# Kernel optimization log

Measured on AMD Instinct MI355X. Metric: run time of the kernel, lower is better.

## Reference

```python
import jax, jax.numpy as jnp
import numpy as np

N_NODES = 150000
N_EDGES = 2400000
F_IN, HID, N_CLS = 22, 32, 6
BN_EPS = 1e-5


def setup_inputs() -> dict:
    key = jax.random.key(0)
    ks = jax.random.split(key, 10)
    x = jax.random.normal(ks[0], (N_NODES, F_IN), dtype=jnp.float32)
    edge_index = jax.random.randint(ks[1], (2, N_EDGES), 0, N_NODES, dtype=jnp.int64)
    # xavier-uniform style linear weights, zero biases (as in _init_weights)
    def xavier(k, fan_in, fan_out):
        lim = float(np.sqrt(6.0 / (fan_in + fan_out)))
        return jax.random.uniform(k, (fan_in, fan_out), jnp.float32, -lim, lim)
    return {
        "x": x,
        "edge_index": edge_index,
        "W_emb": xavier(ks[2], F_IN, HID),
        "b_emb": jnp.zeros((HID,), jnp.float32),
        "W_gcn": xavier(ks[3], HID, HID),
        "b_gcn": jnp.zeros((HID,), jnp.float32),
        "gamma": jnp.ones((HID,), jnp.float32),
        "beta": jnp.zeros((HID,), jnp.float32),
        "W_cls": xavier(ks[4], HID, N_CLS),
        "b_cls": jnp.zeros((N_CLS,), jnp.float32),
    }


def reference(x, edge_index, W_emb, b_emb, W_gcn, b_gcn, gamma, beta, W_cls, b_cls):
    N = x.shape[0]
    # embedding + relu
    h = jax.nn.relu(x @ W_emb + b_emb)                      # [N, HID]
    # GCNConv: linear transform first
    h = h @ W_gcn                                           # [N, HID]
    # add self-loops
    loops = jnp.arange(N, dtype=edge_index.dtype)
    src = jnp.concatenate([edge_index[0], loops])           # [E+N]
    dst = jnp.concatenate([edge_index[1], loops])
    # symmetric normalization deg^{-1/2} A_hat deg^{-1/2}
    deg = jax.ops.segment_sum(jnp.ones_like(dst, dtype=h.dtype), dst, num_segments=N)
    dis = jnp.where(deg > 0, jax.lax.rsqrt(jnp.where(deg > 0, deg, 1.0)), 0.0)
    norm = dis[src] * dis[dst]                              # [E+N]
    msg = h[src] * norm[:, None]                            # gather + scale
    agg = jax.ops.segment_sum(msg, dst, num_segments=N) + b_gcn
    # BatchNorm1d (training-mode batch statistics, biased variance)
    mean = jnp.mean(agg, axis=0)
    var = jnp.mean((agg - mean) ** 2, axis=0)
    hn = (agg - mean) * jax.lax.rsqrt(var + BN_EPS) * gamma + beta
    hn = jax.nn.relu(hn)
    # dropout is identity in eval; classifier
    return hn @ W_cls + b_cls
```

## Files before the change

kernel.cpp:

```cpp
#include <hip/hip_runtime.h>

#define N_NODES 150000
#define N_EDGES 2400000
#define F_IN    22
#define HID     32
#define N_CLS   6
#define BN_EPS  1e-5f

#define BSHIFT  8
#define BMASK   255
#define NB      ((N_NODES + BMASK) >> BSHIFT)
#define NBLK_BIN 256
#define CHUNK   ((N_EDGES + NBLK_BIN - 1) / NBLK_BIN)
#define CHUNK_H 8192
#define NBLK_H  ((N_EDGES + CHUNK_H - 1) / CHUNK_H)
#define EMB_NPB 64
#define NBLK_EMB ((N_NODES + EMB_NPB - 1) / EMB_NPB)
#define NREP    8

__device__ __forceinline__ unsigned bf16rne(float f) {
    unsigned u = __float_as_uint(f);
    return (u + 0x7FFFu + ((u >> 16) & 1u)) >> 16;
}
__device__ __forceinline__ float bflo(unsigned p) { return __uint_as_float(p << 16); }
__device__ __forceinline__ float bfhi(unsigned p) { return __uint_as_float(p & 0xFFFF0000u); }

__global__ void embed_hist_kernel(const float* __restrict__ x,
                                  const float* __restrict__ W_emb,
                                  const float* __restrict__ b_emb,
                                  const float* __restrict__ W_gcn,
                                  unsigned* __restrict__ hb,
                                  const int* __restrict__ dst,
                                  int* __restrict__ bcnt) {
    if (blockIdx.x < NBLK_EMB) {
        __shared__ float sWe[F_IN * HID];
        __shared__ float sbe[HID];
        __shared__ float sWg[HID * HID];
        __shared__ float sx[EMB_NPB * 23];
        __shared__ float sh1[EMB_NPB * 33];
        __shared__ unsigned sp[EMB_NPB * 17];
        for (int t = threadIdx.x; t < F_IN * HID; t += 256) sWe[t] = W_emb[t];
        if (threadIdx.x < HID) sbe[threadIdx.x] = b_emb[threadIdx.x];
        for (int t = threadIdx.x; t < HID * HID; t += 256) sWg[t] = W_gcn[t];

        int nbase = blockIdx.x * EMB_NPB;
        int nvalid = N_NODES - nbase; if (nvalid > EMB_NPB) nvalid = EMB_NPB;

        {
            const float* xg = x + (size_t)nbase * F_IN;
            int totalx = nvalid * F_IN;
            for (int L = threadIdx.x; L < totalx; L += 256)
                sx[(L / F_IN) * 23 + (L % F_IN)] = xg[L];
        }
        __syncthreads();

        int n = threadIdx.x >> 2;
        int q = threadIdx.x & 3;
        bool act = n < nvalid;

        if (act) {
#pragma unroll
            for (int j = 0; j < 8; ++j) {
                float acc = sbe[q * 8 + j];
#pragma unroll
                for (int f = 0; f < F_IN; ++f)
                    acc = fmaf(sx[n * 23 + f], sWe[f * HID + q * 8 + j], acc);
                sh1[n * 33 + q * 8 + j] = fmaxf(acc, 0.0f);
            }
        }
        __syncthreads();

        if (act) {
            float o[8];
#pragma unroll
            for (int j = 0; j < 8; ++j) o[j] = 0.0f;
#pragma unroll
            for (int f = 0; f < HID; ++f) {
                float hv = sh1[n * 33 + f];
#pragma unroll
                for (int j = 0; j < 8; ++j)
                    o[j] = fmaf(hv, sWg[f * HID + q * 8 + j], o[j]);
            }
#pragma unroll
            for (int jj = 0; jj < 4; ++jj)
                sp[n * 17 + q * 4 + jj] = bf16rne(o[2 * jj]) | (bf16rne(o[2 * jj + 1]) << 16);
        }
        __syncthreads();

        int total = nvalid * 16;
        size_t gbase = (size_t)nbase * 16;
        for (int L = threadIdx.x; L < total; L += 256)
            hb[gbase + L] = sp[(L >> 4) * 17 + (L & 15)];
    } else {
        __shared__ int hloc[NB];
        for (int t = threadIdx.x; t < NB; t += 256) hloc[t] = 0;
        __syncthreads();
        int base = (blockIdx.x - NBLK_EMB) * CHUNK_H;
        int end = base + CHUNK_H; if (end > N_EDGES) end = N_EDGES;
        for (int i = base + threadIdx.x; i < end; i += 256)
            atomicAdd(&hloc[dst[i] >> BSHIFT], 1);
        __syncthreads();
        for (int t = threadIdx.x; t < NB; t += 256)
            if (hloc[t]) atomicAdd(&bcnt[t], hloc[t]);
    }
}

__global__ void bucket_scan_kernel(const int* __restrict__ bcnt,
                                   int* __restrict__ boff,
                                   int* __restrict__ bcur,
                                   float* __restrict__ stats) {
    int t = threadIdx.x;
    if (t < 64 * NREP) stats[t] = 0.0f;
    __shared__ int s[1024];
    int v0 = (t < NB) ? bcnt[t] : 0;
    s[t] = v0;
    __syncthreads();
#pragma unroll
    for (int o = 1; o < 1024; o <<= 1) {
        int v = (t >= o) ? s[t - o] : 0;
        __syncthreads();
        s[t] += v;
        __syncthreads();
    }
    if (t < NB) {
        int e = s[t] - v0;
        boff[t] = e;
        bcur[t] = e;
    }
    if (t == NB - 1) boff[NB] = s[t];
}

__global__ void bin_edges_kernel(const int* __restrict__ src,
                                 const int* __restrict__ dst,
                                 int* __restrict__ bcur,
                                 unsigned int* __restrict__ binned) {
    __shared__ int hloc[NB];
    __shared__ int base[NB];
    __shared__ int lcur[NB];
    for (int t = threadIdx.x; t < NB; t += 512) hloc[t] = 0;
    __syncthreads();

    int cbase = blockIdx.x * CHUNK;
    int cend = cbase + CHUNK; if (cend > N_EDGES) cend = N_EDGES;
    for (int i = cbase + threadIdx.x; i < cend; i += 512)
        atomicAdd(&hloc[dst[i] >> BSHIFT], 1);
    __syncthreads();
    for (int t = threadIdx.x; t < NB; t += 512) {
        int c = hloc[t];
        base[t] = c ? atomicAdd(&bcur[t], c) : 0;
        lcur[t] = 0;
    }
    __syncthreads();
    for (int i = cbase + threadIdx.x; i < cend; i += 512) {
        int d = dst[i];
        int b = d >> BSHIFT;
        int r = atomicAdd(&lcur[b], 1);
        binned[base[b] + r] = ((unsigned)(d & BMASK) << 24) | (unsigned)src[i];
    }
}

__global__ void bucket_csr_kernel(const int* __restrict__ boff,
                                  const unsigned int* __restrict__ binned,
                                  int* __restrict__ sorted_src,
                                  int* __restrict__ off,
                                  float* __restrict__ dis) {
    __shared__ int s_cnt[256];
    __shared__ int s_scan[256];
    __shared__ int s_cur[256];
    int b = blockIdx.x;
    int t = threadIdx.x;
    int s0 = boff[b], s1 = boff[b + 1];
    int nbase = b << BSHIFT;
    int nnode = N_NODES - nbase; if (nnode > 256) nnode = 256;

    s_cnt[t] = 0;
    __syncthreads();
    for (int k = s0 + t; k < s1; k += 256)
        atomicAdd(&s_cnt[binned[k] >> 24], 1);
    __syncthreads();

    int v = s_cnt[t];
    s_scan[t] = v;
    __syncthreads();
#pragma unroll
    for (int o = 1; o < 256; o <<= 1) {
        int u = (t >= o) ? s_scan[t - o] : 0;
        __syncthreads();
        s_scan[t] += u;
        __syncthreads();
    }
    int excl = s_scan[t] - v;
    s_cur[t] = excl;
    if (t < nnode) {
        off[nbase + t] = s0 + excl;
        dis[nbase + t] = rsqrtf(1.0f + (float)v);
    }
    if (b == NB - 1 && t == 0) off[N_NODES] = N_EDGES;
    __syncthreads();

    for (int k = s0 + t; k < s1; k += 256) {
        unsigned p = binned[k];
        int n = (int)(p >> 24);
        int r = atomicAdd(&s_cur[n], 1);
        sorted_src[s0 + r] = (int)(p & 0xFFFFFFu);
    }
}

__global__ void aggregate_kernel(const int* __restrict__ off,
                                 const int* __restrict__ sorted_src,
                                 const unsigned* __restrict__ hb,
                                 const float* __restrict__ dis,
                                 float* __restrict__ agg,
                                 float* __restrict__ stats) {
    int t = blockIdx.x * blockDim.x + threadIdx.x;
    int node = t >> 3;
    int c = t & 7;
    bool active = node < N_NODES;

    float4 ps = {0.f, 0.f, 0.f, 0.f};
    float4 pq = {0.f, 0.f, 0.f, 0.f};

    if (active) {
        const uint2* hrow = reinterpret_cast<const uint2*>(hb);
        float dn = dis[node];
        uint2 hp = hrow[(size_t)node * 8 + c];
        float4 a0, a1, a2, a3;
        a0.x = bflo(hp.x) * dn; a0.y = bfhi(hp.x) * dn;
        a0.z = bflo(hp.y) * dn; a0.w = bfhi(hp.y) * dn;
        a1 = a2 = a3 = make_float4(0.f, 0.f, 0.f, 0.f);

        int b = off[node], e = off[node + 1];
        int k = b;
        for (; k + 8 <= e; k += 8) {
            int s0 = sorted_src[k],     s1 = sorted_src[k + 1];
            int s2 = sorted_src[k + 2], s3 = sorted_src[k + 3];
            int s4 = sorted_src[k + 4], s5 = sorted_src[k + 5];
            int s6 = sorted_src[k + 6], s7 = sorted_src[k + 7];
            float d0 = dis[s0], d1 = dis[s1], d2 = dis[s2], d3 = dis[s3];
            float d4 = dis[s4], d5 = dis[s5], d6 = dis[s6], d7 = dis[s7];
            uint2 v0 = hrow[(size_t)s0 * 8 + c];
            uint2 v1 = hrow[(size_t)s1 * 8 + c];
            uint2 v2 = hrow[(size_t)s2 * 8 + c];
            uint2 v3 = hrow[(size_t)s3 * 8 + c];
            uint2 v4 = hrow[(size_t)s4 * 8 + c];
            uint2 v5 = hrow[(size_t)s5 * 8 + c];
            uint2 v6 = hrow[(size_t)s6 * 8 + c];
            uint2 v7 = hrow[(size_t)s7 * 8 + c];
            a0.x = fmaf(bflo(v0.x), d0, a0.x); a0.y = fmaf(bfhi(v0.x), d0, a0.y);
            a0.z = fmaf(bflo(v0.y), d0, a0.z); a0.w = fmaf(bfhi(v0.y), d0, a0.w);
            a1.x = fmaf(bflo(v1.x), d1, a1.x); a1.y = fmaf(bfhi(v1.x), d1, a1.y);
            a1.z = fmaf(bflo(v1.y), d1, a1.z); a1.w = fmaf(bfhi(v1.y), d1, a1.w);
            a2.x = fmaf(bflo(v2.x), d2, a2.x); a2.y = fmaf(bfhi(v2.x), d2, a2.y);
            a2.z = fmaf(bflo(v2.y), d2, a2.z); a2.w = fmaf(bfhi(v2.y), d2, a2.w);
            a3.x = fmaf(bflo(v3.x), d3, a3.x); a3.y = fmaf(bfhi(v3.x), d3, a3.y);
            a3.z = fmaf(bflo(v3.y), d3, a3.z); a3.w = fmaf(bfhi(v3.y), d3, a3.w);
            a0.x = fmaf(bflo(v4.x), d4, a0.x); a0.y = fmaf(bfhi(v4.x), d4, a0.y);
            a0.z = fmaf(bflo(v4.y), d4, a0.z); a0.w = fmaf(bfhi(v4.y), d4, a0.w);
            a1.x = fmaf(bflo(v5.x), d5, a1.x); a1.y = fmaf(bfhi(v5.x), d5, a1.y);
            a1.z = fmaf(bflo(v5.y), d5, a1.z); a1.w = fmaf(bfhi(v5.y), d5, a1.w);
            a2.x = fmaf(bflo(v6.x), d6, a2.x); a2.y = fmaf(bfhi(v6.x), d6, a2.y);
            a2.z = fmaf(bflo(v6.y), d6, a2.z); a2.w = fmaf(bfhi(v6.y), d6, a2.w);
            a3.x = fmaf(bflo(v7.x), d7, a3.x); a3.y = fmaf(bfhi(v7.x), d7, a3.y);
            a3.z = fmaf(bflo(v7.y), d7, a3.z); a3.w = fmaf(bfhi(v7.y), d7, a3.w);
        }
        for (; k < e; ++k) {
            int s = sorted_src[k];
            float d = dis[s];
            uint2 v = hrow[(size_t)s * 8 + c];
            a0.x = fmaf(bflo(v.x), d, a0.x); a0.y = fmaf(bfhi(v.x), d, a0.y);
            a0.z = fmaf(bflo(v.y), d, a0.z); a0.w = fmaf(bfhi(v.y), d, a0.w);
        }
        float4 o;
        o.x = (a0.x + a1.x + a2.x + a3.x) * dn;
        o.y = (a0.y + a1.y + a2.y + a3.y) * dn;
        o.z = (a0.z + a1.z + a2.z + a3.z) * dn;
        o.w = (a0.w + a1.w + a2.w + a3.w) * dn;
        reinterpret_cast<float4*>(agg)[(size_t)node * 8 + c] = o;
        ps = o;
        pq.x = o.x * o.x; pq.y = o.y * o.y; pq.z = o.z * o.z; pq.w = o.w * o.w;
    }

    __shared__ float S[256 * 4];
    __shared__ float Q[256 * 4];
    S[threadIdx.x * 4 + 0] = ps.x; S[threadIdx.x * 4 + 1] = ps.y;
    S[threadIdx.x * 4 + 2] = ps.z; S[threadIdx.x * 4 + 3] = ps.w;
    Q[threadIdx.x * 4 + 0] = pq.x; Q[threadIdx.x * 4 + 1] = pq.y;
    Q[threadIdx.x * 4 + 2] = pq.z; Q[threadIdx.x * 4 + 3] = pq.w;
    __syncthreads();
    if (threadIdx.x < 32) {
        int cc = threadIdx.x >> 2, j = threadIdx.x & 3;
        float s = 0.0f, q = 0.0f;
#pragma unroll
        for (int w = 0; w < 32; ++w) {
            int tid = (w << 3) | cc;
            s += S[tid * 4 + j];
            q += Q[tid * 4 + j];
        }
        float* rep = stats + 64 * (blockIdx.x & (NREP - 1));
        atomicAdd(&rep[threadIdx.x], s);
        atomicAdd(&rep[32 + threadIdx.x], q);
    }
}

__global__ void cls_kernel(const float* __restrict__ agg,
                           const float* __restrict__ stats,
                           const float* __restrict__ gamma,
                           const float* __restrict__ beta,
                           const float* __restrict__ W_cls,
                           const float* __restrict__ b_cls,
                           float* __restrict__ out) {
    __shared__ float sA[HID];
    __shared__ float sB[HID];
    __shared__ float sW[HID * N_CLS];
    __shared__ float sb[N_CLS];
    if (threadIdx.x < HID) {
        float sum = 0.0f, sq = 0.0f;
#pragma unroll
        for (int r = 0; r < NREP; ++r) {
            sum += stats[r * 64 + threadIdx.x];
            sq  += stats[r * 64 + 32 + threadIdx.x];
        }
        const float invN = 1.0f / (float)N_NODES;
        float mean = sum * invN;
        float var = sq * invN - mean * mean;
        float inv = rsqrtf(var + BN_EPS);
        float A = gamma[threadIdx.x] * inv;
        sA[threadIdx.x] = A;
        sB[threadIdx.x] = beta[threadIdx.x] - mean * A;
    }
    for (int t = threadIdx.x; t < HID * N_CLS; t += blockDim.x) sW[t] = W_cls[t];
    if (threadIdx.x < N_CLS) sb[threadIdx.x] = b_cls[threadIdx.x];
    __syncthreads();

    int i = blockIdx.x * blockDim.x + threadIdx.x;
    if (i >= N_NODES) return;

    float acc[N_CLS];
#pragma unroll
    for (int c = 0; c < N_CLS; ++c) acc[c] = sb[c];
#pragma unroll
    for (int f = 0; f < HID; ++f) {
        float t = fmaxf(fmaf(agg[(size_t)i * HID + f], sA[f], sB[f]), 0.0f);
#pragma unroll
        for (int c = 0; c < N_CLS; ++c) acc[c] = fmaf(t, sW[f * N_CLS + c], acc[c]);
    }
#pragma unroll
    for (int c = 0; c < N_CLS; ++c) out[(size_t)i * N_CLS + c] = acc[c];
}

extern "C" void kernel_launch(void* const* d_in, const int* in_sizes, int n_in,
                              void* d_out, int out_size, void* d_ws, size_t ws_size,
                              hipStream_t stream) {
    const float* x     = (const float*)d_in[0];
    const int*   edge  = (const int*)d_in[1];
    const float* W_emb = (const float*)d_in[2];
    const float* b_emb = (const float*)d_in[3];
    const float* W_gcn = (const float*)d_in[4];
    const float* gamma = (const float*)d_in[6];
    const float* beta  = (const float*)d_in[7];
    const float* W_cls = (const float*)d_in[8];
    const float* b_cls = (const float*)d_in[9];
    float* out = (float*)d_out;

    unsigned*     hb         = (unsigned*)d_ws;
    float*        agg        = (float*)(hb + (size_t)N_NODES * HID / 2);
    float*        dis        = agg + (size_t)N_NODES * HID;
    int*          off        = (int*)(dis + N_NODES);
    int*          bcnt       = off + N_NODES + 1;
    int*          boff       = bcnt + NB;
    int*          bcur       = boff + NB + 1;
    unsigned int* binned     = (unsigned int*)(bcur + NB);
    int*          sorted_src = (int*)(binned + N_EDGES);
    float*        stats      = (float*)(sorted_src + N_EDGES);

    hipMemsetAsync(bcnt, 0, NB * sizeof(int), stream);

    const int* src = edge;
    const int* dst = edge + N_EDGES;

    embed_hist_kernel<<<NBLK_EMB + NBLK_H, 256, 0, stream>>>(x, W_emb, b_emb, W_gcn,
                                                             hb, dst, bcnt);
    bucket_scan_kernel<<<1, 1024, 0, stream>>>(bcnt, boff, bcur, stats);
    bin_edges_kernel<<<NBLK_BIN, 512, 0, stream>>>(src, dst, bcur, binned);
    bucket_csr_kernel<<<NB, 256, 0, stream>>>(boff, binned, sorted_src, off, dis);
    aggregate_kernel<<<(N_NODES * 8 + 255) / 256, 256, 0, stream>>>(off, sorted_src,
                                                                    hb, dis, agg, stats);
    cls_kernel<<<(N_NODES + 255) / 256, 256, 0, stream>>>(agg, stats, gamma, beta,
                                                          W_cls, b_cls, out);
}
```

Measured before the change: 154.0 us.

## Prescale bf16 features by source degree norm and prefetch neighbor indices

Each source row of the bf16 hidden features is multiplied once by its deg^-1/2 inside the CSR bucketing kernel, so the aggregation loop no longer gathers dis[src] per edge. The inner loop becomes plain adds. Neighbor indices for the next group of eight edges are software-prefetched so their loads overlap the current row gathers. The trade-off is an extra bf16 rounding of the scaled features and an extra read-modify-write pass over hb.

After: 150.0 us. 1.03x faster.

```diff
diff --git a/kernel.cpp b/kernel.cpp
--- a/kernel.cpp
+++ b/kernel.cpp
@@ -163,10 +163,12 @@
                                   const unsigned int* __restrict__ binned,
                                   int* __restrict__ sorted_src,
                                   int* __restrict__ off,
-                                  float* __restrict__ dis) {
+                                  float* __restrict__ dis,
+                                  unsigned* __restrict__ hb) {
     __shared__ int s_cnt[256];
     __shared__ int s_scan[256];
     __shared__ int s_cur[256];
+    __shared__ float dl[256];
     int b = blockIdx.x;
     int t = threadIdx.x;
     int s0 = boff[b], s1 = boff[b + 1];
@@ -191,9 +193,11 @@
     }
     int excl = s_scan[t] - v;
     s_cur[t] = excl;
+    float d = rsqrtf(1.0f + (float)v);
+    dl[t] = d;
     if (t < nnode) {
         off[nbase + t] = s0 + excl;
-        dis[nbase + t] = rsqrtf(1.0f + (float)v);
+        dis[nbase + t] = d;
     }
     if (b == NB - 1 && t == 0) off[N_NODES] = N_EDGES;
     __syncthreads();
@@ -203,6 +207,15 @@
         int n = (int)(p >> 24);
         int r = atomicAdd(&s_cur[n], 1);
         sorted_src[s0 + r] = (int)(p & 0xFFFFFFu);
+    }
+
+    uint2* hv = reinterpret_cast<uint2*>(hb) + (size_t)nbase * 8;
+    for (int tt = t; tt < nnode * 8; tt += 256) {
+        uint2 w = hv[tt];
+        float dd = dl[tt >> 3];
+        w.x = bf16rne(bflo(w.x) * dd) | (bf16rne(bfhi(w.x) * dd) << 16);
+        w.y = bf16rne(bflo(w.y) * dd) | (bf16rne(bfhi(w.y) * dd) << 16);
+        hv[tt] = w;
     }
 }
 
@@ -225,50 +238,55 @@
         float dn = dis[node];
         uint2 hp = hrow[(size_t)node * 8 + c];
         float4 a0, a1, a2, a3;
-        a0.x = bflo(hp.x) * dn; a0.y = bfhi(hp.x) * dn;
-        a0.z = bflo(hp.y) * dn; a0.w = bfhi(hp.y) * dn;
+        a0.x = bflo(hp.x); a0.y = bfhi(hp.x);
+        a0.z = bflo(hp.y); a0.w = bfhi(hp.y);
         a1 = a2 = a3 = make_float4(0.f, 0.f, 0.f, 0.f);
 
-        int b = off[node], e = off[node + 1];
-        int k = b;
-        for (; k + 8 <= e; k += 8) {
-            int s0 = sorted_src[k],     s1 = sorted_src[k + 1];
-            int s2 = sorted_src[k + 2], s3 = sorted_src[k + 3];
-            int s4 = sorted_src[k + 4], s5 = sorted_src[k + 5];
-            int s6 = sorted_src[k + 6], s7 = sorted_src[k + 7];
-            float d0 = dis[s0], d1 = dis[s1], d2 = dis[s2], d3 = dis[s3];
-            float d4 = dis[s4], d5 = dis[s5], d6 = dis[s6], d7 = dis[s7];
-            uint2 v0 = hrow[(size_t)s0 * 8 + c];
-            uint2 v1 = hrow[(size_t)s1 * 8 + c];
-            uint2 v2 = hrow[(size_t)s2 * 8 + c];
-            uint2 v3 = hrow[(size_t)s3 * 8 + c];
-            uint2 v4 = hrow[(size_t)s4 * 8 + c];
-            uint2 v5 = hrow[(size_t)s5 * 8 + c];
-            uint2 v6 = hrow[(size_t)s6 * 8 + c];
-            uint2 v7 = hrow[(size_t)s7 * 8 + c];
-            a0.x = fmaf(bflo(v0.x), d0, a0.x); a0.y = fmaf(bfhi(v0.x), d0, a0.y);
-            a0.z = fmaf(bflo(v0.y), d0, a0.z); a0.w = fmaf(bfhi(v0.y), d0, a0.w);
-            a1.x = fmaf(bflo(v1.x), d1, a1.x); a1.y = fmaf(bfhi(v1.x), d1, a1.y);
-            a1.z = fmaf(bflo(v1.y), d1, a1.z); a1.w = fmaf(bfhi(v1.y), d1, a1.w);
-            a2.x = fmaf(bflo(v2.x), d2, a2.x); a2.y = fmaf(bfhi(v2.x), d2, a2.y);
-            a2.z = fmaf(bflo(v2.y), d2, a2.z); a2.w = fmaf(bfhi(v2.y), d2, a2.w);
-            a3.x = fmaf(bflo(v3.x), d3, a3.x); a3.y = fmaf(bfhi(v3.x), d3, a3.y);
-            a3.z = fmaf(bflo(v3.y), d3, a3.z); a3.w = fmaf(bfhi(v3.y), d3, a3.w);
-            a0.x = fmaf(bflo(v4.x), d4, a0.x); a0.y = fmaf(bfhi(v4.x), d4, a0.y);
-            a0.z = fmaf(bflo(v4.y), d4, a0.z); a0.w = fmaf(bfhi(v4.y), d4, a0.w);
-            a1.x = fmaf(bflo(v5.x), d5, a1.x); a1.y = fmaf(bfhi(v5.x), d5, a1.y);
-            a1.z = fmaf(bflo(v5.y), d5, a1.z); a1.w = fmaf(bfhi(v5.y), d5, a1.w);
-            a2.x = fmaf(bflo(v6.x), d6, a2.x); a2.y = fmaf(bfhi(v6.x), d6, a2.y);
-            a2.z = fmaf(bflo(v6.y), d6, a2.z); a2.w = fmaf(bfhi(v6.y), d6, a2.w);
-            a3.x = fmaf(bflo(v7.x), d7, a3.x); a3.y = fmaf(bfhi(v7.x), d7, a3.y);
-            a3.z = fmaf(bflo(v7.y), d7, a3.z); a3.w = fmaf(bfhi(v7.y), d7, a3.w);
-        }
-        for (; k < e; ++k) {
+        int b0 = off[node], e0 = off[node + 1];
+        int cnt8 = (e0 - b0) >> 3;
+        int k = b0;
+        int p0 = 0, p1 = 0, p2 = 0, p3 = 0, p4 = 0, p5 = 0, p6 = 0, p7 = 0;
+        if (cnt8 > 0) {
+            p0 = sorted_src[k];     p1 = sorted_src[k + 1];
+            p2 = sorted_src[k + 2]; p3 = sorted_src[k + 3];
+            p4 = sorted_src[k + 4]; p5 = sorted_src[k + 5];
+            p6 = sorted_src[k + 6]; p7 = sorted_src[k + 7];
+        }
+        for (int it = 0; it < cnt8; ++it) {
+            int kn = k + 8;
+            int n0 = p0, n1 = p1, n2 = p2, n3 = p3;
+            int n4 = p4, n5 = p5, n6 = p6, n7 = p7;
+            if (it + 1 < cnt8) {
+                n0 = sorted_src[kn];     n1 = sorted_src[kn + 1];
+                n2 = sorted_src[kn + 2]; n3 = sorted_src[kn + 3];
+                n4 = sorted_src[kn + 4]; n5 = sorted_src[kn + 5];
+                n6 = sorted_src[kn + 6]; n7 = sorted_src[kn + 7];
+            }
+            uint2 v0 = hrow[(size_t)p0 * 8 + c];
+            uint2 v1 = hrow[(size_t)p1 * 8 + c];
+            uint2 v2 = hrow[(size_t)p2 * 8 + c];
+            uint2 v3 = hrow[(size_t)p3 * 8 + c];
+            uint2 v4 = hrow[(size_t)p4 * 8 + c];
+            uint2 v5 = hrow[(size_t)p5 * 8 + c];
+            uint2 v6 = hrow[(size_t)p6 * 8 + c];
+            uint2 v7 = hrow[(size_t)p7 * 8 + c];
+            a0.x += bflo(v0.x); a0.y += bfhi(v0.x); a0.z += bflo(v0.y); a0.w += bfhi(v0.y);
+            a1.x += bflo(v1.x); a1.y += bfhi(v1.x); a1.z += bflo(v1.y); a1.w += bfhi(v1.y);
+            a2.x += bflo(v2.x); a2.y += bfhi(v2.x); a2.z += bflo(v2.y); a2.w += bfhi(v2.y);
+            a3.x += bflo(v3.x); a3.y += bfhi(v3.x); a3.z += bflo(v3.y); a3.w += bfhi(v3.y);
+            a0.x += bflo(v4.x); a0.y += bfhi(v4.x); a0.z += bflo(v4.y); a0.w += bfhi(v4.y);
+            a1.x += bflo(v5.x); a1.y += bfhi(v5.x); a1.z += bflo(v5.y); a1.w += bfhi(v5.y);
+            a2.x += bflo(v6.x); a2.y += bfhi(v6.x); a2.z += bflo(v6.y); a2.w += bfhi(v6.y);
+            a3.x += bflo(v7.x); a3.y += bfhi(v7.x); a3.z += bflo(v7.y); a3.w += bfhi(v7.y);
+            p0 = n0; p1 = n1; p2 = n2; p3 = n3;
+            p4 = n4; p5 = n5; p6 = n6; p7 = n7;
+            k = kn;
+        }
+        for (; k < e0; ++k) {
             int s = sorted_src[k];
-            float d = dis[s];
             uint2 v = hrow[(size_t)s * 8 + c];
-            a0.x = fmaf(bflo(v.x), d, a0.x); a0.y = fmaf(bfhi(v.x), d, a0.y);
-            a0.z = fmaf(bflo(v.y), d, a0.z); a0.w = fmaf(bfhi(v.y), d, a0.w);
+            a0.x += bflo(v.x); a0.y += bfhi(v.x);
+            a0.z += bflo(v.y); a0.w += bfhi(v.y);
         }
         float4 o;
         o.x = (a0.x + a1.x + a2.x + a3.x) * dn;
@@ -382,7 +400,7 @@
                                                              hb, dst, bcnt);
     bucket_scan_kernel<<<1, 1024, 0, stream>>>(bcnt, boff, bcur, stats);
     bin_edges_kernel<<<NBLK_BIN, 512, 0, stream>>>(src, dst, bcur, binned);
-    bucket_csr_kernel<<<NB, 256, 0, stream>>>(boff, binned, sorted_src, off, dis);
+    bucket_csr_kernel<<<NB, 256, 0, stream>>>(boff, binned, sorted_src, off, dis, hb);
     aggregate_kernel<<<(N_NODES * 8 + 255) / 256, 256, 0, stream>>>(off, sorted_src,
                                                                     hb, dis, agg, stats);
     cls_kernel<<<(N_NODES + 255) / 256, 256, 0, stream>>>(agg, stats, gamma, beta,
```
